# Optimization experiments

Measured on AMD Instinct MI355X. Metric: run time of the kernel, lower is better.

The kernel has to match this reference:

```python
import jax, jax.numpy as jnp
import numpy as np


def setup_inputs() -> dict:
    key = jax.random.key(0)
    k1, k2, k3 = jax.random.split(key, 3)
    B, N, D = 8, 4096, 64
    q = jax.random.normal(k1, (B, N, D), dtype=jnp.float32)
    k = jax.random.normal(k2, (B, N, D), dtype=jnp.float32)
    v = jax.random.normal(k3, (B, N, D), dtype=jnp.float32)
    attn_mask = jnp.ones((B, N), dtype=jnp.int32)  # 1 = attend, 0 = padding
    return {"q": q, "k": k, "v": v, "attn_mask": attn_mask}


def reference(q, k, v, attn_mask):
    # q: [B, n_q, d], k/v: [B, n_k, d], attn_mask: [B, n_k]
    d = q.shape[-1]
    n_q, n_k = q.shape[1], k.shape[1]
    scale = jnp.sqrt(jnp.asarray(d, dtype=q.dtype))
    # [B, n_q, n_k] attention logits
    logits = jnp.einsum("bqd,bkd->bqk", q, k) / scale
    # causal (mask_future=True): tril keep-mask over (n_q, n_k)
    causal = jnp.tril(jnp.ones((n_q, n_k), dtype=bool))
    neg_inf = jnp.asarray(-jnp.inf, dtype=logits.dtype)
    logits = jnp.where(causal[None, :, :], logits, neg_inf)
    # padding mask broadcast over query dim: [B, 1, n_k]
    logits = jnp.where(attn_mask[:, None, :] == 0, neg_inf, logits)
    w = jax.nn.softmax(logits, axis=-1)
    return jnp.einsum("bqk,bkd->bqd", w, v)
```

## Files before the change

### kernel.cpp

```cpp
#include <hip/hip_runtime.h>


#define BATCH 8
#define SEQ   4096
#define DIM   64
#define NKT   (SEQ / 64)

typedef __attribute__((ext_vector_type(8)))  short bf16x8;
typedef __attribute__((ext_vector_type(16))) float f32x16;

__device__ inline short f2bf(float f) {
    unsigned u = __builtin_bit_cast(unsigned, f);
    u += 0x7FFFu + ((u >> 16) & 1u);
    return (short)(u >> 16);
}
__device__ inline unsigned pk2bf(float a, float b) {
    unsigned ua = __builtin_bit_cast(unsigned, a) + 0x8000u;
    unsigned ub = __builtin_bit_cast(unsigned, b) + 0x8000u;
    return __builtin_amdgcn_perm(ub, ua, 0x07060302u);
}
__device__ inline float fast_exp2(float x) {
#if __has_builtin(__builtin_amdgcn_exp2f)
    return __builtin_amdgcn_exp2f(x);
#else
    return exp2f(x);
#endif
}
__device__ inline bf16x8 pack8(const float4& a, const float4& b) {
    bf16x8 r;
    r[0] = f2bf(a.x); r[1] = f2bf(a.y); r[2] = f2bf(a.z); r[3] = f2bf(a.w);
    r[4] = f2bf(b.x); r[5] = f2bf(b.y); r[6] = f2bf(b.z); r[7] = f2bf(b.w);
    return r;
}
__device__ inline void gl_lds16(const void* g, void* l) {
    __builtin_amdgcn_global_load_lds(
        (const __attribute__((address_space(1))) void*)g,
        (__attribute__((address_space(3))) void*)l, 16, 0, 0);
}

__global__ __launch_bounds__(256)
void prep_kv(const float* __restrict__ kg, const float* __restrict__ vg,
             short* __restrict__ kw, short* __restrict__ vw) {
    const int tile = blockIdx.x;
    const float* kp = kg + (size_t)tile * 64 * DIM;
    const float* vp = vg + (size_t)tile * 64 * DIM;
    short* ko = kw + (size_t)tile * 4096;
    short* vo = vw + (size_t)tile * 4096;
    const int t = threadIdx.x;
#pragma unroll
    for (int i = 0; i < 4; ++i) {
        const int flat = i * 256 + t;
        const int key = flat >> 4, d0 = (flat & 15) * 4;
        const float4 kv = *(const float4*)(kp + (size_t)key * DIM + d0);
        uint2 kpk;
        kpk.x = pk2bf(kv.x, kv.y); kpk.y = pk2bf(kv.z, kv.w);
        *(uint2*)(ko + (((d0 >> 3) << 6) + key) * 8 + (d0 & 7)) = kpk;
        const float4 vv = *(const float4*)(vp + (size_t)key * DIM + d0);
        const int kc = key >> 3, jk = key & 7;
        vo[((kc << 6) + d0 + 0) * 8 + jk] = f2bf(vv.x);
        vo[((kc << 6) + d0 + 1) * 8 + jk] = f2bf(vv.y);
        vo[((kc << 6) + d0 + 2) * 8 + jk] = f2bf(vv.z);
        vo[((kc << 6) + d0 + 3) * 8 + jk] = f2bf(vv.w);
    }
}

template <bool WS>
__global__ __launch_bounds__(256, 2)
void attn_fwd(const float* __restrict__ qg, const float* __restrict__ kg,
              const float* __restrict__ vg, const int* __restrict__ mg,
              float* __restrict__ og, const short* __restrict__ kw,
              const short* __restrict__ vw) {
    __shared__ __align__(16) char smem[33024];
    short* KbS = (short*)smem;
    short* VbS = (short*)(smem + 16384);
    float* Lb  = (float*)(smem + 32768);
    float* ObF = (float*)smem;

    const int t    = threadIdx.x;
    const int w    = t >> 6;
    const int L    = t & 63;
    const int q31  = L & 31;
    const int h    = L >> 5;
    const int kh   = w & 1;
    const int qsub = w >> 1;

    const int id = blockIdx.x;
    const int b  = id & 7;
    const int j  = id >> 3;
    const int qb = (j & 1) ? (j >> 1) : (63 - (j >> 1));
    const int qbase  = qb * 64;
    const int ntiles = qb + 1;

    const float* qp = qg + (size_t)b * SEQ * DIM;
    const float* kp = kg + (size_t)b * SEQ * DIM;
    const float* vp = vg + (size_t)b * SEQ * DIM;
    const int*   mp = mg + (size_t)b * SEQ;
    const short* kwb = WS ? kw + (size_t)b * NKT * 4096 : nullptr;
    const short* vwb = WS ? vw + (size_t)b * NKT * 4096 : nullptr;

    const int qrow = qbase + qsub * 32 + q31;
    const float qscale = 0.125f * 1.44269504088896340736f;

    bf16x8 Qf[4];
#pragma unroll
    for (int c = 0; c < 4; ++c) {
        const float* src = qp + (size_t)qrow * DIM + c * 16 + h * 8;
        float4 x = *(const float4*)src;
        float4 y = *(const float4*)(src + 4);
        x.x *= qscale; x.y *= qscale; x.z *= qscale; x.w *= qscale;
        y.x *= qscale; y.y *= qscale; y.z *= qscale; y.w *= qscale;
        Qf[c] = pack8(x, y);
    }

    auto stage = [&](int bs, int kt) {
        const short* ks = kwb + (size_t)kt * 4096;
        const short* vs = vwb + (size_t)kt * 4096;
#pragma unroll
        for (int it = 0; it < 2; ++it) {
            const int off = (w << 10) + (it << 9);
            gl_lds16(ks + off + (L << 3), KbS + bs * 4096 + off);
            gl_lds16(vs + off + (L << 3), VbS + bs * 4096 + off);
        }
    };

    float lsum = 0.0f;
    f32x16 Oacc[2];
#pragma unroll
    for (int nb = 0; nb < 2; ++nb)
#pragma unroll
        for (int r = 0; r < 16; ++r) Oacc[nb][r] = 0.0f;

    if constexpr (WS) stage(0, 0);

    for (int kt = 0; kt < ntiles; ++kt) {
        const int cur = WS ? (kt & 1) : 0;

        if constexpr (WS) {
            __syncthreads();
            if (kt + 1 < ntiles) stage(cur ^ 1, kt + 1);
        } else {
            __syncthreads();
#pragma unroll
            for (int i = 0; i < 4; ++i) {
                const int flat = i * 256 + t;
                const int key = flat >> 4, d0 = (flat & 15) * 4;
                const float4 kv = *(const float4*)(kp + (size_t)(kt * 64 + key) * DIM + d0);
                uint2 kk;
                kk.x = pk2bf(kv.x, kv.y); kk.y = pk2bf(kv.z, kv.w);
                *(uint2*)&KbS[(((d0 >> 3) << 6) + key) * 8 + (d0 & 7)] = kk;
                const float4 vv = *(const float4*)(vp + (size_t)(kt * 64 + key) * DIM + d0);
                const int kc = key >> 3, jk = key & 7;
                VbS[((kc << 6) + d0 + 0) * 8 + jk] = f2bf(vv.x);
                VbS[((kc << 6) + d0 + 1) * 8 + jk] = f2bf(vv.y);
                VbS[((kc << 6) + d0 + 2) * 8 + jk] = f2bf(vv.z);
                VbS[((kc << 6) + d0 + 3) * 8 + jk] = f2bf(vv.w);
            }
            __syncthreads();
        }

        const short* Kt = KbS + cur * 4096;
        const short* Vt = VbS + cur * 4096;

        int4 Md[4];
#pragma unroll
        for (int g = 0; g < 4; ++g)
            Md[g] = *(const int4*)&mp[kt * 64 + kh * 32 + 8 * g + 4 * h];

        f32x16 sa;
#pragma unroll
        for (int r = 0; r < 16; ++r) sa[r] = 0.0f;
#pragma unroll
        for (int c = 0; c < 4; ++c) {
            bf16x8 kf = *(const bf16x8*)&Kt[(((2 * c + h) << 6) + kh * 32 + q31) * 8];
            sa = __builtin_amdgcn_mfma_f32_32x32x16_bf16(kf, Qf[c], sa, 0, 0, 0);
        }

        const bool diag = (kt == ntiles - 1);
        float p[16];
#pragma unroll
        for (int g = 0; g < 4; ++g) {
            const int mi[4] = {Md[g].x, Md[g].y, Md[g].z, Md[g].w};
#pragma unroll
            for (int e = 0; e < 4; ++e) {
                const int reg = g * 4 + e;
                float s = sa[reg];
                bool keep = (mi[e] != 0);
                if (diag) {
                    const int keyg = kt * 64 + kh * 32 + 4 * h + 8 * g + e;
                    keep = keep && (keyg <= qrow);
                }
                s = keep ? s : -1e30f;
                p[reg] = fast_exp2(fminf(s, 80.0f));
                lsum += p[reg];
            }
        }

        unsigned u[8], su[8];
#pragma unroll
        for (int i = 0; i < 8; ++i) u[i] = pk2bf(p[2 * i], p[2 * i + 1]);
#pragma unroll
        for (int i = 0; i < 8; ++i) su[i] = (unsigned)__shfl_xor((int)u[i], 32);
        int4 fi0 = h ? (int4){(int)su[2], (int)su[3], (int)u[2], (int)u[3]}
                     : (int4){(int)u[0], (int)u[1], (int)su[0], (int)su[1]};
        int4 fi1 = h ? (int4){(int)su[6], (int)su[7], (int)u[6], (int)u[7]}
                     : (int4){(int)u[4], (int)u[5], (int)su[4], (int)su[5]};
        bf16x8 pf0 = __builtin_bit_cast(bf16x8, fi0);
        bf16x8 pf1 = __builtin_bit_cast(bf16x8, fi1);

#pragma unroll
        for (int kk = 0; kk < 2; ++kk) {
            const bf16x8 pf = kk ? pf1 : pf0;
#pragma unroll
            for (int nb = 0; nb < 2; ++nb) {
                bf16x8 vf = *(const bf16x8*)&Vt[(((4 * kh + 2 * kk + h) << 6) + nb * 32 + q31) * 8];
                Oacc[nb] = __builtin_amdgcn_mfma_f32_32x32x16_bf16(vf, pf, Oacc[nb], 0, 0, 0);
            }
        }
    }

    lsum += __shfl_xor(lsum, 32);

    __syncthreads();
    float* Ob = ObF + qsub * 2080;
    if (kh == 1) {
#pragma unroll
        for (int nb = 0; nb < 2; ++nb)
#pragma unroll
            for (int r = 0; r < 16; ++r)
                Ob[((nb * 16 + r) * 2 + h) * 32 + q31] = Oacc[nb][r];
        if (h == 0) Lb[qsub * 32 + q31] = lsum;
    }
    __syncthreads();
    if (kh == 0) {
        const float inv = 1.0f / (lsum + Lb[qsub * 32 + q31]);
#pragma unroll
        for (int nb = 0; nb < 2; ++nb)
#pragma unroll
            for (int r = 0; r < 16; ++r)
                Oacc[nb][r] = (Oacc[nb][r] + Ob[((nb * 16 + r) * 2 + h) * 32 + q31]) * inv;
#pragma unroll
        for (int nb = 0; nb < 2; ++nb)
#pragma unroll
            for (int g = 0; g < 4; ++g)
#pragma unroll
                for (int e = 0; e < 4; ++e) {
                    const int d = nb * 32 + 4 * h + 8 * g + e;
                    Ob[q31 * 65 + d] = Oacc[nb][g * 4 + e];
                }
        float* op = og + (size_t)b * SEQ * DIM;
#pragma unroll
        for (int i = 0; i < 8; ++i) {
            const int flat = i * 256 + (L << 2);
            const int row = flat >> 6, d = flat & 63;
            const float4 val = *(const float4*)&Ob[row * 65 + d];
            *(float4*)&op[(size_t)(qbase + qsub * 32 + row) * DIM + d] = val;
        }
    }
}

extern "C" void kernel_launch(void* const* d_in, const int* in_sizes, int n_in,
                              void* d_out, int out_size, void* d_ws, size_t ws_size,
                              hipStream_t stream) {
    (void)in_sizes; (void)n_in; (void)out_size;
    const float* q = (const float*)d_in[0];
    const float* k = (const float*)d_in[1];
    const float* v = (const float*)d_in[2];
    const int*   m = (const int*)d_in[3];
    float* o = (float*)d_out;
    const size_t need = (size_t)BATCH * NKT * 4096 * sizeof(short) * 2;
    if (ws_size >= need) {
        short* kw = (short*)d_ws;
        short* vw = kw + (size_t)BATCH * NKT * 4096;
        prep_kv<<<dim3(BATCH * NKT), 256, 0, stream>>>(k, v, kw, vw);
        attn_fwd<true><<<dim3(512), 256, 0, stream>>>(q, k, v, m, o, kw, vw);
    } else {
        attn_fwd<false><<<dim3(512), 256, 0, stream>>>(q, k, v, m, o, nullptr, nullptr);
    }
}
```

Before: 141.0 us.

## Double workgroup to 512 threads, splitting key tiles across two wave groups

Each workgroup now runs eight waves. Two groups of four each process alternating 64-key tiles, so every loop step stages two K/V tiles (doubled LDS buffers). The partial outputs and row sums from the extra waves are combined in shared memory through a four-way reduction, and the results are written straight to global memory. The aim is to halve the serial loop trip count per query block and raise MFMA parallelism. The cost is larger LDS use per block, a heavier final reduction, and idle waves on odd tile counts.

Measured after the change: 144.5 us. 1.02x slower.

```diff
diff --git a/kernel.cpp b/kernel.cpp
--- a/kernel.cpp
+++ b/kernel.cpp
@@ -65,15 +65,15 @@
 }
 
 template <bool WS>
-__global__ __launch_bounds__(256, 2)
+__global__ __launch_bounds__(512, 4)
 void attn_fwd(const float* __restrict__ qg, const float* __restrict__ kg,
               const float* __restrict__ vg, const int* __restrict__ mg,
               float* __restrict__ og, const short* __restrict__ kw,
               const short* __restrict__ vw) {
-    __shared__ __align__(16) char smem[33024];
+    __shared__ __align__(16) char smem[66560];
     short* KbS = (short*)smem;
-    short* VbS = (short*)(smem + 16384);
-    float* Lb  = (float*)(smem + 32768);
+    short* VbS = (short*)(smem + 32768);
+    float* Lb  = (float*)(smem + 65536);
     float* ObF = (float*)smem;
 
     const int t    = threadIdx.x;
@@ -81,8 +81,9 @@
     const int L    = t & 63;
     const int q31  = L & 31;
     const int h    = L >> 5;
-    const int kh   = w & 1;
-    const int qsub = w >> 1;
+    const int qsub = w & 1;
+    const int kh   = (w >> 1) & 1;
+    const int tp   = w >> 2;
 
     const int id = blockIdx.x;
     const int b  = id & 7;
@@ -90,6 +91,7 @@
     const int qb = (j & 1) ? (j >> 1) : (63 - (j >> 1));
     const int qbase  = qb * 64;
     const int ntiles = qb + 1;
+    const int nss    = (ntiles + 1) >> 1;
 
     const float* qp = qg + (size_t)b * SEQ * DIM;
     const float* kp = kg + (size_t)b * SEQ * DIM;
@@ -112,14 +114,14 @@
         Qf[c] = pack8(x, y);
     }
 
-    auto stage = [&](int bs, int kt) {
-        const short* ks = kwb + (size_t)kt * 4096;
-        const short* vs = vwb + (size_t)kt * 4096;
+    auto stage = [&](int bs, int pp) {
+        const short* ks = kwb + (size_t)pp * 8192;
+        const short* vs = vwb + (size_t)pp * 8192;
 #pragma unroll
         for (int it = 0; it < 2; ++it) {
             const int off = (w << 10) + (it << 9);
-            gl_lds16(ks + off + (L << 3), KbS + bs * 4096 + off);
-            gl_lds16(vs + off + (L << 3), VbS + bs * 4096 + off);
+            gl_lds16(ks + off + (L << 3), KbS + bs * 8192 + off);
+            gl_lds16(vs + off + (L << 3), VbS + bs * 8192 + off);
         }
     };
 
@@ -132,129 +134,137 @@
 
     if constexpr (WS) stage(0, 0);
 
-    for (int kt = 0; kt < ntiles; ++kt) {
-        const int cur = WS ? (kt & 1) : 0;
+    for (int ss = 0; ss < nss; ++ss) {
+        const int cur = WS ? (ss & 1) : 0;
 
         if constexpr (WS) {
             __syncthreads();
-            if (kt + 1 < ntiles) stage(cur ^ 1, kt + 1);
+            if (ss + 1 < nss) stage(cur ^ 1, ss + 1);
         } else {
             __syncthreads();
 #pragma unroll
             for (int i = 0; i < 4; ++i) {
-                const int flat = i * 256 + t;
-                const int key = flat >> 4, d0 = (flat & 15) * 4;
-                const float4 kv = *(const float4*)(kp + (size_t)(kt * 64 + key) * DIM + d0);
+                const int flat = i * 512 + t;
+                const int tl = flat >> 10;
+                const int rem = flat & 1023;
+                const int key = rem >> 4, d0 = (rem & 15) * 4;
+                const size_t row = (size_t)((2 * ss + tl) * 64 + key);
+                const float4 kv = *(const float4*)(kp + row * DIM + d0);
                 uint2 kk;
                 kk.x = pk2bf(kv.x, kv.y); kk.y = pk2bf(kv.z, kv.w);
-                *(uint2*)&KbS[(((d0 >> 3) << 6) + key) * 8 + (d0 & 7)] = kk;
-                const float4 vv = *(const float4*)(vp + (size_t)(kt * 64 + key) * DIM + d0);
+                *(uint2*)&KbS[tl * 4096 + (((d0 >> 3) << 6) + key) * 8 + (d0 & 7)] = kk;
+                const float4 vv = *(const float4*)(vp + row * DIM + d0);
                 const int kc = key >> 3, jk = key & 7;
-                VbS[((kc << 6) + d0 + 0) * 8 + jk] = f2bf(vv.x);
-                VbS[((kc << 6) + d0 + 1) * 8 + jk] = f2bf(vv.y);
-                VbS[((kc << 6) + d0 + 2) * 8 + jk] = f2bf(vv.z);
-                VbS[((kc << 6) + d0 + 3) * 8 + jk] = f2bf(vv.w);
+                VbS[tl * 4096 + ((kc << 6) + d0 + 0) * 8 + jk] = f2bf(vv.x);
+                VbS[tl * 4096 + ((kc << 6) + d0 + 1) * 8 + jk] = f2bf(vv.y);
+                VbS[tl * 4096 + ((kc << 6) + d0 + 2) * 8 + jk] = f2bf(vv.z);
+                VbS[tl * 4096 + ((kc << 6) + d0 + 3) * 8 + jk] = f2bf(vv.w);
             }
             __syncthreads();
         }
 
-        const short* Kt = KbS + cur * 4096;
-        const short* Vt = VbS + cur * 4096;
-
-        int4 Md[4];
-#pragma unroll
-        for (int g = 0; g < 4; ++g)
-            Md[g] = *(const int4*)&mp[kt * 64 + kh * 32 + 8 * g + 4 * h];
-
-        f32x16 sa;
-#pragma unroll
-        for (int r = 0; r < 16; ++r) sa[r] = 0.0f;
-#pragma unroll
-        for (int c = 0; c < 4; ++c) {
-            bf16x8 kf = *(const bf16x8*)&Kt[(((2 * c + h) << 6) + kh * 32 + q31) * 8];
-            sa = __builtin_amdgcn_mfma_f32_32x32x16_bf16(kf, Qf[c], sa, 0, 0, 0);
+        const int tile = 2 * ss + tp;
+        if (tile < ntiles) {
+            const short* Kt = KbS + cur * 8192 + tp * 4096;
+            const short* Vt = VbS + cur * 8192 + tp * 4096;
+
+            int4 Md[4];
+#pragma unroll
+            for (int g = 0; g < 4; ++g)
+                Md[g] = *(const int4*)&mp[tile * 64 + kh * 32 + 8 * g + 4 * h];
+
+            f32x16 sa;
+#pragma unroll
+            for (int r = 0; r < 16; ++r) sa[r] = 0.0f;
+#pragma unroll
+            for (int c = 0; c < 4; ++c) {
+                bf16x8 kf = *(const bf16x8*)&Kt[(((2 * c + h) << 6) + kh * 32 + q31) * 8];
+                sa = __builtin_amdgcn_mfma_f32_32x32x16_bf16(kf, Qf[c], sa, 0, 0, 0);
+            }
+
+            const bool diag = (tile == ntiles - 1);
+            float p[16];
+#pragma unroll
+            for (int g = 0; g < 4; ++g) {
+                const int mi[4] = {Md[g].x, Md[g].y, Md[g].z, Md[g].w};
+#pragma unroll
+                for (int e = 0; e < 4; ++e) {
+                    const int reg = g * 4 + e;
+                    float s = sa[reg];
+                    bool keep = (mi[e] != 0);
+                    if (diag) {
+                        const int keyg = tile * 64 + kh * 32 + 4 * h + 8 * g + e;
+                        keep = keep && (keyg <= qrow);
+                    }
+                    s = keep ? s : -1e30f;
+                    p[reg] = fast_exp2(fminf(s, 80.0f));
+                    lsum += p[reg];
+                }
+            }
+
+            unsigned u[8], su[8];
+#pragma unroll
+            for (int i = 0; i < 8; ++i) u[i] = pk2bf(p[2 * i], p[2 * i + 1]);
+#pragma unroll
+            for (int i = 0; i < 8; ++i) su[i] = (unsigned)__shfl_xor((int)u[i], 32);
+            int4 fi0 = h ? (int4){(int)su[2], (int)su[3], (int)u[2], (int)u[3]}
+                         : (int4){(int)u[0], (int)u[1], (int)su[0], (int)su[1]};
+            int4 fi1 = h ? (int4){(int)su[6], (int)su[7], (int)u[6], (int)u[7]}
+                         : (int4){(int)u[4], (int)u[5], (int)su[4], (int)su[5]};
+            bf16x8 pf0 = __builtin_bit_cast(bf16x8, fi0);
+            bf16x8 pf1 = __builtin_bit_cast(bf16x8, fi1);
+
+#pragma unroll
+            for (int kk = 0; kk < 2; ++kk) {
+                const bf16x8 pf = kk ? pf1 : pf0;
+#pragma unroll
+                for (int nb = 0; nb < 2; ++nb) {
+                    bf16x8 vf = *(const bf16x8*)&Vt[(((4 * kh + 2 * kk + h) << 6) + nb * 32 + q31) * 8];
+                    Oacc[nb] = __builtin_amdgcn_mfma_f32_32x32x16_bf16(vf, pf, Oacc[nb], 0, 0, 0);
+                }
+            }
         }
-
-        const bool diag = (kt == ntiles - 1);
-        float p[16];
-#pragma unroll
-        for (int g = 0; g < 4; ++g) {
-            const int mi[4] = {Md[g].x, Md[g].y, Md[g].z, Md[g].w};
-#pragma unroll
-            for (int e = 0; e < 4; ++e) {
-                const int reg = g * 4 + e;
-                float s = sa[reg];
-                bool keep = (mi[e] != 0);
-                if (diag) {
-                    const int keyg = kt * 64 + kh * 32 + 4 * h + 8 * g + e;
-                    keep = keep && (keyg <= qrow);
-                }
-                s = keep ? s : -1e30f;
-                p[reg] = fast_exp2(fminf(s, 80.0f));
-                lsum += p[reg];
-            }
-        }
-
-        unsigned u[8], su[8];
-#pragma unroll
-        for (int i = 0; i < 8; ++i) u[i] = pk2bf(p[2 * i], p[2 * i + 1]);
-#pragma unroll
-        for (int i = 0; i < 8; ++i) su[i] = (unsigned)__shfl_xor((int)u[i], 32);
-        int4 fi0 = h ? (int4){(int)su[2], (int)su[3], (int)u[2], (int)u[3]}
-                     : (int4){(int)u[0], (int)u[1], (int)su[0], (int)su[1]};
-        int4 fi1 = h ? (int4){(int)su[6], (int)su[7], (int)u[6], (int)u[7]}
-                     : (int4){(int)u[4], (int)u[5], (int)su[4], (int)su[5]};
-        bf16x8 pf0 = __builtin_bit_cast(bf16x8, fi0);
-        bf16x8 pf1 = __builtin_bit_cast(bf16x8, fi1);
-
-#pragma unroll
-        for (int kk = 0; kk < 2; ++kk) {
-            const bf16x8 pf = kk ? pf1 : pf0;
-#pragma unroll
-            for (int nb = 0; nb < 2; ++nb) {
-                bf16x8 vf = *(const bf16x8*)&Vt[(((4 * kh + 2 * kk + h) << 6) + nb * 32 + q31) * 8];
-                Oacc[nb] = __builtin_amdgcn_mfma_f32_32x32x16_bf16(vf, pf, Oacc[nb], 0, 0, 0);
-            }
-        }
     }
 
     lsum += __shfl_xor(lsum, 32);
 
     __syncthreads();
-    float* Ob = ObF + qsub * 2080;
-    if (kh == 1) {
+    if (w >= 2) {
+        const int r = ((w - 2) >> 1) + qsub * 3;
+        float* Ow = ObF + r * 2048;
 #pragma unroll
         for (int nb = 0; nb < 2; ++nb)
 #pragma unroll
-            for (int r = 0; r < 16; ++r)
-                Ob[((nb * 16 + r) * 2 + h) * 32 + q31] = Oacc[nb][r];
-        if (h == 0) Lb[qsub * 32 + q31] = lsum;
+            for (int g = 0; g < 4; ++g)
+#pragma unroll
+                for (int e = 0; e < 4; ++e)
+                    Ow[(nb * 32 + 4 * h + 8 * g + e) * 32 + q31] = Oacc[nb][g * 4 + e];
+        if (h == 0) Lb[w * 32 + q31] = lsum;
     }
     __syncthreads();
-    if (kh == 0) {
-        const float inv = 1.0f / (lsum + Lb[qsub * 32 + q31]);
+    if (w < 2) {
+        const int s = w;
+        const float ltot = lsum + Lb[(s + 2) * 32 + q31] + Lb[(s + 4) * 32 + q31]
+                                + Lb[(s + 6) * 32 + q31];
+        const float inv = 1.0f / ltot;
+        const float* R0 = ObF + (s * 3 + 0) * 2048;
+        const float* R1 = ObF + (s * 3 + 1) * 2048;
+        const float* R2 = ObF + (s * 3 + 2) * 2048;
+        float* op = og + (size_t)b * SEQ * DIM + (size_t)(qbase + s * 32 + q31) * DIM;
 #pragma unroll
         for (int nb = 0; nb < 2; ++nb)
 #pragma unroll
-            for (int r = 0; r < 16; ++r)
-                Oacc[nb][r] = (Oacc[nb][r] + Ob[((nb * 16 + r) * 2 + h) * 32 + q31]) * inv;
-#pragma unroll
-        for (int nb = 0; nb < 2; ++nb)
-#pragma unroll
-            for (int g = 0; g < 4; ++g)
+            for (int g = 0; g < 4; ++g) {
+                float4 v4;
+                float* vv = (float*)&v4;
 #pragma unroll
                 for (int e = 0; e < 4; ++e) {
                     const int d = nb * 32 + 4 * h + 8 * g + e;
-                    Ob[q31 * 65 + d] = Oacc[nb][g * 4 + e];
+                    vv[e] = (Oacc[nb][g * 4 + e] + R0[d * 32 + q31] + R1[d * 32 + q31]
+                             + R2[d * 32 + q31]) * inv;
                 }
-        float* op = og + (size_t)b * SEQ * DIM;
-#pragma unroll
-        for (int i = 0; i < 8; ++i) {
-            const int flat = i * 256 + (L << 2);
-            const int row = flat >> 6, d = flat & 63;
-            const float4 val = *(const float4*)&Ob[row * 65 + d];
-            *(float4*)&op[(size_t)(qbase + qsub * 32 + row) * DIM + d] = val;
-        }
+                *(float4*)&op[nb * 32 + 4 * h + 8 * g] = v4;
+            }
     }
 }
 
@@ -272,8 +282,8 @@
         short* kw = (short*)d_ws;
         short* vw = kw + (size_t)BATCH * NKT * 4096;
         prep_kv<<<dim3(BATCH * NKT), 256, 0, stream>>>(k, v, kw, vw);
-        attn_fwd<true><<<dim3(512), 256, 0, stream>>>(q, k, v, m, o, kw, vw);
+        attn_fwd<true><<<dim3(512), 512, 0, stream>>>(q, k, v, m, o, kw, vw);
     } else {
-        attn_fwd<false><<<dim3(512), 256, 0, stream>>>(q, k, v, m, o, nullptr, nullptr);
-    }
-}
+        attn_fwd<false><<<dim3(512), 512, 0, stream>>>(q, k, v, m, o, nullptr, nullptr);
+    }
+}
```
